# Kernel optimization log

Hardware: AMD Instinct MI355X
Metric: run time of the kernel (lower is better)

## Reference

```python
import jax, jax.numpy as jnp
import numpy as np

B, C, H, W = 8, 256, 128, 128
K = 3  # conv kernel size, padding=1 -> SAME


def conv3x3(x, w, b):
    # x: [B,C,H,W], w: [O,I,K,K], b: [O]
    y = jax.lax.conv_general_dilated(
        x, w, window_strides=(1, 1), padding='SAME',
        dimension_numbers=('NCHW', 'OIHW', 'NCHW'))
    return y + b[None, :, None, None]


def setup_inputs() -> dict:
    key = jax.random.key(0)
    ks = jax.random.split(key, 7)
    fan_in = C * K * K
    s = 1.0 / np.sqrt(fan_in)
    x = jax.random.normal(ks[0], (B, C, H, W), dtype=jnp.float32)
    Wq = jax.random.uniform(ks[1], (C, C, K, K), jnp.float32, -s, s)
    bq = jax.random.uniform(ks[2], (C,), jnp.float32, -s, s)
    Wk = jax.random.uniform(ks[3], (C, C, K, K), jnp.float32, -s, s)
    bk = jax.random.uniform(ks[4], (C,), jnp.float32, -s, s)
    Wv = jax.random.uniform(ks[5], (C, C, K, K), jnp.float32, -s, s)
    bv = jax.random.uniform(ks[6], (C,), jnp.float32, -s, s)
    return {'x': x, 'Wq': Wq, 'bq': bq, 'Wk': Wk, 'bk': bk, 'Wv': Wv, 'bv': bv}


def reference(x, Wq, bq, Wk, bk, Wv, bv):
    b_, c_, h_, w_ = x.shape
    residual = x
    q = jax.nn.relu(conv3x3(x, Wq, bq))  # [B,C,H,W]
    k = jax.nn.relu(conv3x3(x, Wk, bk))  # [B,C,H,W]
    v = conv3x3(x, Wv, bv)               # [B,C,H,W]
    # per-(batch,channel) spatial matmul: [H,W] @ [H,W] -> [H,W] (requires H==W)
    attn = jnp.einsum('bcij,bcjk->bcik', q, k)
    # softmax over the flattened H*W positions jointly per (b,c)
    attn = jax.nn.softmax(attn.reshape(b_, c_, h_ * w_), axis=-1).reshape(b_, c_, h_, w_)
    y = jnp.einsum('bcij,bcjk->bcik', attn, v)
    return y + residual
```

## Files before the change

### kernel.cpp

```cpp
#include <hip/hip_runtime.h>

#define BB 8
#define CC 256
#define HH 128
#define WW 128
#define HW (HH*WW)

typedef float f32x4 __attribute__((ext_vector_type(4)));
typedef float f32x16 __attribute__((ext_vector_type(16)));
typedef short s16x8 __attribute__((ext_vector_type(8)));

__device__ inline unsigned short f2bf(float f) {
  union { float f; unsigned int u; } un;
  un.f = f;
  unsigned int u = un.u;
  return (unsigned short)((u + 0x7fffu + ((u >> 16) & 1u)) >> 16);
}

__device__ __forceinline__ void gload_lds16(const void* g, void* l) {
  __builtin_amdgcn_global_load_lds(
      (const __attribute__((address_space(1))) unsigned int*)g,
      (__attribute__((address_space(3))) unsigned int*)l, 16, 0, 0);
}

__global__ __launch_bounds__(256) void k_prepass(const float* __restrict__ x,
                                                 unsigned short* __restrict__ xbf) {
  __shared__ float tile[64][68];
  int bh = blockIdx.x;
  int b = bh >> 7, h = bh & 127;
  int w0 = blockIdx.y * 64;
  int c0 = blockIdx.z * 64;
  int t = threadIdx.x;
  {
    int c = t >> 2, wq = (t & 3) << 4;
    const float4* src = reinterpret_cast<const float4*>(
        x + (((size_t)(b * CC + c0 + c) * HH + h) * WW + w0 + wq));
    float4 v0 = src[0], v1 = src[1], v2 = src[2], v3 = src[3];
    *reinterpret_cast<float4*>(&tile[c][wq + 0])  = v0;
    *reinterpret_cast<float4*>(&tile[c][wq + 4])  = v1;
    *reinterpret_cast<float4*>(&tile[c][wq + 8])  = v2;
    *reinterpret_cast<float4*>(&tile[c][wq + 12]) = v3;
  }
  __syncthreads();
  {
    int w = t >> 2, cg = (t & 3) << 4;
    unsigned short tmp[16];
#pragma unroll
    for (int i = 0; i < 16; ++i) tmp[i] = f2bf(tile[cg + i][w]);
    unsigned short* dst = xbf + ((size_t)(b * HH + h) * WW + w0 + w) * CC + c0 + cg;
    *reinterpret_cast<int4*>(dst)     = *reinterpret_cast<int4*>(tmp);
    *reinterpret_cast<int4*>(dst + 8) = *reinterpret_cast<int4*>(tmp + 8);
  }
}

__global__ __launch_bounds__(256) void k_repack(const float* __restrict__ Wq,
                                                const float* __restrict__ Wk,
                                                const float* __restrict__ Wv,
                                                unsigned short* __restrict__ Wp,
                                                unsigned short* __restrict__ zp) {
  if (blockIdx.x == 0 && threadIdx.x < 64) {
    int4 z = {0, 0, 0, 0};
    reinterpret_cast<int4*>(zp)[threadIdx.x] = z;
  }
  int idx = blockIdx.x * 256 + threadIdx.x;
  if (idx >= 8 * 9 * 768 * 32) return;
  int ci = idx & 31;
  int tmp = idx >> 5;
  int focs = tmp % 768;
  int tmp2 = tmp / 768;
  int tap = tmp2 % 9;
  int chunk = tmp2 / 9;
  int cv = focs >> 8, oc = focs & 255;
  int cin = chunk * 32 + ci;
  const float* Wsrc = (cv == 0) ? Wq : ((cv == 1) ? Wk : Wv);
  Wp[idx] = f2bf(Wsrc[(size_t)(oc * 256 + cin) * 9 + tap]);
}

__global__ __launch_bounds__(256, 2) void k_conv(const unsigned short* __restrict__ xbf,
                                                 const unsigned short* __restrict__ Wp,
                                                 const unsigned short* __restrict__ zp,
                                                 const float* __restrict__ bq,
                                                 const float* __restrict__ bk,
                                                 const float* __restrict__ bv,
                                                 unsigned short* __restrict__ qkv) {
  __shared__ unsigned short xs[2][4][132][32];
  __shared__ float bias_s[128];
  int bid = blockIdx.x;
  int v_ = (bid & 7) * 384 + (bid >> 3);
  int mtile = v_ % 6;
  int bhp = v_ / 6;
  int b = bhp >> 6;
  int h0 = (bhp & 63) * 2;
  int t = threadIdx.x;
  int lane = t & 63, wave = t >> 6;
  int wm = wave >> 1, wq = wave & 1;
  int l31 = lane & 31, lg1 = lane >> 5;

  if (t < 128) {
    int focs = mtile * 128 + t;
    int cv = focs >> 8, oc = focs & 255;
    const float* bp = (cv == 0) ? bq : ((cv == 1) ? bk : bv);
    bias_s[t] = bp[oc];
  }
  {
    int cell = t >> 4;
    int bf_ = cell >> 3, r_ = (cell >> 1) & 3;
    int wc_ = (cell & 1) ? 129 : 0;
    *reinterpret_cast<int*>(reinterpret_cast<char*>(&xs[bf_][r_][wc_][0]) + (t & 15) * 4) = 0;
  }

  int l2 = lane >> 2, l4 = lane & 3;
  int osw = l4 ^ (((l2 + 1) >> 1) & 3);
  int hin = h0 + wave - 1;
  bool inb = ((unsigned)hin < 128u);
  const unsigned short* srow =
      xbf + ((size_t)(b * HH + (inb ? hin : 0)) * WW + l2) * CC + osw * 8;
  const unsigned short* zsrc = zp + lane * 8;

  const size_t CH_STRIDE = (size_t)9 * 768 * 32;
  const unsigned short* apbase = Wp + (size_t)(mtile * 128 + wm * 64 + l31) * 32 + lg1 * 8;

  f32x16 acc[2][2][2] = {};
  s16x8 Afb[2][3][2];

  {
    char* d0 = reinterpret_cast<char*>(&xs[0][wave][1][0]);
    if (inb) {
#pragma unroll
      for (int j = 0; j < 8; ++j) gload_lds16(srow + j * (16 * CC), d0 + j * 1024);
    } else {
#pragma unroll
      for (int j = 0; j < 8; ++j) gload_lds16(zsrc, d0 + j * 1024);
    }
  }
#pragma unroll
  for (int rr = 0; rr < 3; ++rr)
#pragma unroll
  for (int mt = 0; mt < 2; ++mt)
    Afb[0][rr][mt] = *reinterpret_cast<const s16x8*>(apbase + (rr * 3) * (768 * 32) + mt * 1024);
  __syncthreads();

  for (int chunk = 0; chunk < 8; ++chunk) {
    const int buf = chunk & 1;
    const unsigned short* ap_cur = apbase + chunk * CH_STRIDE;
    const unsigned short* ap_nxt = (chunk < 7) ? ap_cur + CH_STRIDE : ap_cur;
    const char* xsb = reinterpret_cast<const char*>(&xs[buf][0][0][0]);
    char* dstg = reinterpret_cast<char*>(&xs[buf ^ 1][wave][1][0]);
    const unsigned short* sstg = srow + (chunk + 1) * 32;

#pragma unroll
    for (int p = 0; p < 6; ++p) {
      const int ss = p >> 1, kk = p & 1;
      s16x8 Bf[4][2];
#pragma unroll
      for (int rin = 0; rin < 4; ++rin)
#pragma unroll
      for (int nt = 0; nt < 2; ++nt) {
        int wc = wq * 64 + nt * 32 + l31 + ss;
        int pslot = (kk * 2 + lg1) ^ ((wc >> 1) & 3);
        Bf[rin][nt] = *reinterpret_cast<const s16x8*>(
            xsb + rin * (132 * 64) + wc * 64 + pslot * 16);
      }
      {
        const int pn = (p + 1) % 6, ssn = pn >> 1, kkn = pn & 1;
        const unsigned short* apn = (p == 5) ? ap_nxt : ap_cur;
#pragma unroll
        for (int rr = 0; rr < 3; ++rr)
#pragma unroll
        for (int mt = 0; mt < 2; ++mt)
          Afb[(p + 1) & 1][rr][mt] = *reinterpret_cast<const s16x8*>(
              apn + (rr * 3 + ssn) * (768 * 32) + mt * 1024 + kkn * 16);
      }
      __builtin_amdgcn_sched_barrier(0);
      if (p < 4 && chunk < 7) {
        if (inb) {
          gload_lds16(sstg + (2 * p) * (16 * CC), dstg + (2 * p) * 1024);
          gload_lds16(sstg + (2 * p + 1) * (16 * CC), dstg + (2 * p + 1) * 1024);
        } else {
          gload_lds16(zsrc, dstg + (2 * p) * 1024);
          gload_lds16(zsrc, dstg + (2 * p + 1) * 1024);
        }
      }
      __builtin_amdgcn_sched_barrier(0);
      __builtin_amdgcn_s_setprio(1);
#pragma unroll
      for (int rr = 0; rr < 3; ++rr)
#pragma unroll
      for (int row = 0; row < 2; ++row)
#pragma unroll
      for (int mt = 0; mt < 2; ++mt)
#pragma unroll
      for (int nt = 0; nt < 2; ++nt)
        acc[mt][row][nt] = __builtin_amdgcn_mfma_f32_32x32x16_bf16(
            Afb[p & 1][rr][mt], Bf[row + rr][nt], acc[mt][row][nt], 0, 0, 0);
      __builtin_amdgcn_s_setprio(0);
      __builtin_amdgcn_sched_barrier(0);
    }
    if (chunk < 7) {
      asm volatile("s_waitcnt vmcnt(12)" ::: "memory");
      __builtin_amdgcn_s_barrier();
      asm volatile("" ::: "memory");
      __builtin_amdgcn_sched_barrier(0);
    }
  }

#pragma unroll
  for (int mt = 0; mt < 2; ++mt) {
#pragma unroll
    for (int row = 0; row < 2; ++row) {
#pragma unroll
      for (int nt = 0; nt < 2; ++nt) {
        int wcol = wq * 64 + nt * 32 + l31;
        int h = h0 + row;
#pragma unroll
        for (int reg = 0; reg < 16; ++reg) {
          int rloc = (reg & 3) + 8 * (reg >> 2) + 4 * lg1;
          int floc = wm * 64 + mt * 32 + rloc;
          float vv = acc[mt][row][nt][reg] + bias_s[floc];
          int focs = mtile * 128 + floc;
          if (focs < 512) vv = fmaxf(vv, 0.0f);
          int cv = focs >> 8, oc = focs & 255;
          qkv[(size_t)(cv * 2048 + b * 256 + oc) * HW + h * WW + wcol] = f2bf(vv);
        }
      }
    }
  }
}

#define PADA 136
__global__ __launch_bounds__(256) void k_attn(const unsigned short* __restrict__ qkv,
                                              const float* __restrict__ x,
                                              float* __restrict__ out) {
  __shared__ unsigned short al[128][PADA];
  __shared__ unsigned short kt[128][PADA];
  __shared__ unsigned short vt[128][PADA];
  __shared__ float red[8];
  int bc = blockIdx.x;
  const unsigned short* qp = qkv + (size_t)bc * HW;
  const unsigned short* kp = qkv + (size_t)(2048 + bc) * HW;
  const unsigned short* vp = qkv + (size_t)(4096 + bc) * HW;
  int t = threadIdx.x;
  for (int g = t; g < HW; g += 256) {
    int row = g >> 7, col = g & 127;
    kt[col][row] = kp[g];
    vt[col][row] = vp[g];
  }
  __syncthreads();
  int lane = t & 63, wave = t >> 6;
  int wm = wave >> 1, wn = wave & 1;
  int l15 = lane & 15, lg = lane >> 4;
  f32x4 acc[4][4] = {};
#pragma unroll
  for (int kk = 0; kk < 4; ++kk) {
    s16x8 af[4], bfr[4];
#pragma unroll
    for (int m = 0; m < 4; ++m)
      af[m] = *reinterpret_cast<const s16x8*>(qp + (size_t)(wm * 64 + m * 16 + l15) * WW + kk * 32 + lg * 8);
#pragma unroll
    for (int n = 0; n < 4; ++n)
      bfr[n] = *reinterpret_cast<const s16x8*>(&kt[wn * 64 + n * 16 + l15][kk * 32 + lg * 8]);
#pragma unroll
    for (int m = 0; m < 4; ++m)
#pragma unroll
      for (int n = 0; n < 4; ++n)
        acc[m][n] = __builtin_amdgcn_mfma_f32_16x16x32_bf16(af[m], bfr[n], acc[m][n], 0, 0, 0);
  }
  float lm = -3.0e38f;
#pragma unroll
  for (int m = 0; m < 4; ++m)
#pragma unroll
    for (int n = 0; n < 4; ++n)
#pragma unroll
      for (int rg = 0; rg < 4; ++rg)
        lm = fmaxf(lm, acc[m][n][rg]);
  for (int off = 32; off > 0; off >>= 1) lm = fmaxf(lm, __shfl_xor(lm, off));
  if (lane == 0) red[wave] = lm;
  __syncthreads();
  float M = fmaxf(fmaxf(red[0], red[1]), fmaxf(red[2], red[3]));
  float ls = 0.0f;
#pragma unroll
  for (int m = 0; m < 4; ++m)
#pragma unroll
    for (int n = 0; n < 4; ++n)
#pragma unroll
      for (int rg = 0; rg < 4; ++rg)
        ls += __expf(acc[m][n][rg] - M);
  for (int off = 32; off > 0; off >>= 1) ls += __shfl_xor(ls, off);
  if (lane == 0) red[4 + wave] = ls;
  __syncthreads();
  float inv = 1.0f / (red[4] + red[5] + red[6] + red[7]);
#pragma unroll
  for (int m = 0; m < 4; ++m) {
#pragma unroll
    for (int n = 0; n < 4; ++n) {
      int col = wn * 64 + n * 16 + l15;
#pragma unroll
      for (int rg = 0; rg < 4; ++rg) {
        int row = wm * 64 + m * 16 + lg * 4 + rg;
        al[row][col] = f2bf(__expf(acc[m][n][rg] - M) * inv);
      }
    }
  }
  __syncthreads();
  f32x4 o_[4][4] = {};
#pragma unroll
  for (int kk = 0; kk < 4; ++kk) {
    s16x8 af[4], bfr[4];
#pragma unroll
    for (int m = 0; m < 4; ++m)
      af[m] = *reinterpret_cast<const s16x8*>(&al[wm * 64 + m * 16 + l15][kk * 32 + lg * 8]);
#pragma unroll
    for (int n = 0; n < 4; ++n)
      bfr[n] = *reinterpret_cast<const s16x8*>(&vt[wn * 64 + n * 16 + l15][kk * 32 + lg * 8]);
#pragma unroll
    for (int m = 0; m < 4; ++m)
#pragma unroll
      for (int n = 0; n < 4; ++n)
        o_[m][n] = __builtin_amdgcn_mfma_f32_16x16x32_bf16(af[m], bfr[n], o_[m][n], 0, 0, 0);
  }
  const float* xp = x + (size_t)bc * HW;
  float* op = out + (size_t)bc * HW;
#pragma unroll
  for (int m = 0; m < 4; ++m) {
#pragma unroll
    for (int n = 0; n < 4; ++n) {
      int col = wn * 64 + n * 16 + l15;
#pragma unroll
      for (int rg = 0; rg < 4; ++rg) {
        int row = wm * 64 + m * 16 + lg * 4 + rg;
        op[row * WW + col] = o_[m][n][rg] + xp[row * WW + col];
      }
    }
  }
}

extern "C" void kernel_launch(void* const* d_in, const int* in_sizes, int n_in,
                              void* d_out, int out_size, void* d_ws, size_t ws_size,
                              hipStream_t stream) {
  const float* x  = (const float*)d_in[0];
  const float* Wq = (const float*)d_in[1];
  const float* bq = (const float*)d_in[2];
  const float* Wk = (const float*)d_in[3];
  const float* bk = (const float*)d_in[4];
  const float* Wv = (const float*)d_in[5];
  const float* bv = (const float*)d_in[6];
  float* out = (float*)d_out;

  unsigned short* xbf = (unsigned short*)d_ws;
  unsigned short* qkv = xbf + (size_t)33554432;
  unsigned short* Wp  = qkv + (size_t)3 * 33554432;
  unsigned short* zp  = Wp + (size_t)(8 * 9 * 768 * 32);

  dim3 g0(1024, 2, 4);
  k_prepass<<<g0, 256, 0, stream>>>(x, xbf);
  k_repack<<<6912, 256, 0, stream>>>(Wq, Wk, Wv, Wp, zp);
  k_conv<<<3072, 256, 0, stream>>>(xbf, Wp, zp, bq, bk, bv, qkv);
  k_attn<<<2048, 256, 0, stream>>>(qkv, x, out);
}
```

Before: 606.1 us.

## Reassign conv waves to 32-filter by full-width tiles with pipelined B-fragment loads

Changes the conv kernel's wave decomposition from a 2x2 grid (64 filters x 64 columns per wave) to 4 waves each owning 32 filters across all 128 columns. Each wave now loads fewer weight fragments and reads more LDS activation fragments, which are software-pipelined one column tile ahead and interleaved with the MFMAs. This aims to cut global weight-load traffic and register pressure and to overlap LDS reads with compute. In exchange LDS read volume per wave rises, and the wait count before each barrier is adjusted.

```diff
diff --git a/kernel.cpp b/kernel.cpp
--- a/kernel.cpp
+++ b/kernel.cpp
@@ -93,7 +93,7 @@
   int h0 = (bhp & 63) * 2;
   int t = threadIdx.x;
   int lane = t & 63, wave = t >> 6;
-  int wm = wave >> 1, wq = wave & 1;
+  int fq = wave;
   int l31 = lane & 31, lg1 = lane >> 5;
 
   if (t < 128) {
@@ -118,110 +118,109 @@
   const unsigned short* zsrc = zp + lane * 8;
 
   const size_t CH_STRIDE = (size_t)9 * 768 * 32;
-  const unsigned short* apbase = Wp + (size_t)(mtile * 128 + wm * 64 + l31) * 32 + lg1 * 8;
-
-  f32x16 acc[2][2][2] = {};
-  s16x8 Afb[2][3][2];
-
-  {
-    char* d0 = reinterpret_cast<char*>(&xs[0][wave][1][0]);
+  const unsigned short* apbase = Wp + (size_t)(mtile * 128 + fq * 32 + l31) * 32 + lg1 * 8;
+
+  auto STAGE = [&](int bufn, int c) {
+    char* d0 = reinterpret_cast<char*>(&xs[bufn][wave][1][0]);
     if (inb) {
-#pragma unroll
-      for (int j = 0; j < 8; ++j) gload_lds16(srow + j * (16 * CC), d0 + j * 1024);
+      const unsigned short* s0 = srow + c * 32;
+#pragma unroll
+      for (int j = 0; j < 8; ++j) gload_lds16(s0 + j * (16 * CC), d0 + j * 1024);
     } else {
 #pragma unroll
       for (int j = 0; j < 8; ++j) gload_lds16(zsrc, d0 + j * 1024);
     }
-  }
-#pragma unroll
-  for (int rr = 0; rr < 3; ++rr)
-#pragma unroll
-  for (int mt = 0; mt < 2; ++mt)
-    Afb[0][rr][mt] = *reinterpret_cast<const s16x8*>(apbase + (rr * 3) * (768 * 32) + mt * 1024);
-  __syncthreads();
+  };
+  auto ALOAD = [&](s16x8 (&Af)[3], const unsigned short* ap, int un) {
+    const int ss = un >> 1, kk = un & 1;
+#pragma unroll
+    for (int rr = 0; rr < 3; ++rr)
+      Af[rr] = *reinterpret_cast<const s16x8*>(ap + (rr * 3 + ss) * (768 * 32) + kk * 16);
+  };
+  auto BREAD = [&](s16x8 (&Bf)[4], const char* xsb, int un, int nt) {
+    const int ss = un >> 1, kk = un & 1;
+    const int col = nt * 32 + l31 + ss;
+    const int pslot = (kk * 2 + lg1) ^ ((col >> 1) & 3);
+#pragma unroll
+    for (int rin = 0; rin < 4; ++rin)
+      Bf[rin] = *reinterpret_cast<const s16x8*>(
+          xsb + rin * (132 * 64) + col * 64 + pslot * 16);
+  };
+
+  f32x16 acc[2][4] = {};
+  s16x8 Afb[2][3];
+  s16x8 Bfb[2][4];
+
+  STAGE(0, 0);
+  ALOAD(Afb[0], apbase, 0);
+  asm volatile("s_waitcnt vmcnt(3)" ::: "memory");
+  __builtin_amdgcn_s_barrier();
+  BREAD(Bfb[0], reinterpret_cast<const char*>(&xs[0][0][0][0]), 0, 0);
 
   for (int chunk = 0; chunk < 8; ++chunk) {
     const int buf = chunk & 1;
     const unsigned short* ap_cur = apbase + chunk * CH_STRIDE;
-    const unsigned short* ap_nxt = (chunk < 7) ? ap_cur + CH_STRIDE : ap_cur;
     const char* xsb = reinterpret_cast<const char*>(&xs[buf][0][0][0]);
-    char* dstg = reinterpret_cast<char*>(&xs[buf ^ 1][wave][1][0]);
-    const unsigned short* sstg = srow + (chunk + 1) * 32;
-
-#pragma unroll
-    for (int p = 0; p < 6; ++p) {
-      const int ss = p >> 1, kk = p & 1;
-      s16x8 Bf[4][2];
-#pragma unroll
-      for (int rin = 0; rin < 4; ++rin)
-#pragma unroll
-      for (int nt = 0; nt < 2; ++nt) {
-        int wc = wq * 64 + nt * 32 + l31 + ss;
-        int pslot = (kk * 2 + lg1) ^ ((wc >> 1) & 3);
-        Bf[rin][nt] = *reinterpret_cast<const s16x8*>(
-            xsb + rin * (132 * 64) + wc * 64 + pslot * 16);
+
+#pragma unroll
+    for (int u = 0; u < 6; ++u) {
+#pragma unroll
+      for (int nt = 0; nt < 4; ++nt) {
+        if (nt < 3) {
+          BREAD(Bfb[(nt + 1) & 1], xsb, u, nt + 1);
+        } else if (u < 5) {
+          BREAD(Bfb[0], xsb, u + 1, 0);
+        }
+        if (nt == 0) {
+          if (u < 5) ALOAD(Afb[(u + 1) & 1], ap_cur, u + 1);
+          else if (chunk < 7) ALOAD(Afb[0], ap_cur + CH_STRIDE, 0);
+          if (u < 4 && chunk < 7) {
+            char* dstg = reinterpret_cast<char*>(&xs[buf ^ 1][wave][1][0]);
+            if (inb) {
+              const unsigned short* s0 = srow + (chunk + 1) * 32;
+              gload_lds16(s0 + (2 * u) * (16 * CC), dstg + (2 * u) * 1024);
+              gload_lds16(s0 + (2 * u + 1) * (16 * CC), dstg + (2 * u + 1) * 1024);
+            } else {
+              gload_lds16(zsrc, dstg + (2 * u) * 1024);
+              gload_lds16(zsrc, dstg + (2 * u + 1) * 1024);
+            }
+          }
+        }
+        __builtin_amdgcn_sched_barrier(0);
+        __builtin_amdgcn_s_setprio(1);
+#pragma unroll
+        for (int rr = 0; rr < 3; ++rr)
+#pragma unroll
+          for (int row = 0; row < 2; ++row)
+            acc[row][nt] = __builtin_amdgcn_mfma_f32_32x32x16_bf16(
+                Afb[u & 1][rr], Bfb[nt & 1][row + rr], acc[row][nt], 0, 0, 0);
+        __builtin_amdgcn_s_setprio(0);
+        __builtin_amdgcn_sched_barrier(0);
       }
-      {
-        const int pn = (p + 1) % 6, ssn = pn >> 1, kkn = pn & 1;
-        const unsigned short* apn = (p == 5) ? ap_nxt : ap_cur;
-#pragma unroll
-        for (int rr = 0; rr < 3; ++rr)
-#pragma unroll
-        for (int mt = 0; mt < 2; ++mt)
-          Afb[(p + 1) & 1][rr][mt] = *reinterpret_cast<const s16x8*>(
-              apn + (rr * 3 + ssn) * (768 * 32) + mt * 1024 + kkn * 16);
-      }
-      __builtin_amdgcn_sched_barrier(0);
-      if (p < 4 && chunk < 7) {
-        if (inb) {
-          gload_lds16(sstg + (2 * p) * (16 * CC), dstg + (2 * p) * 1024);
-          gload_lds16(sstg + (2 * p + 1) * (16 * CC), dstg + (2 * p + 1) * 1024);
-        } else {
-          gload_lds16(zsrc, dstg + (2 * p) * 1024);
-          gload_lds16(zsrc, dstg + (2 * p + 1) * 1024);
-        }
-      }
-      __builtin_amdgcn_sched_barrier(0);
-      __builtin_amdgcn_s_setprio(1);
-#pragma unroll
-      for (int rr = 0; rr < 3; ++rr)
-#pragma unroll
-      for (int row = 0; row < 2; ++row)
-#pragma unroll
-      for (int mt = 0; mt < 2; ++mt)
-#pragma unroll
-      for (int nt = 0; nt < 2; ++nt)
-        acc[mt][row][nt] = __builtin_amdgcn_mfma_f32_32x32x16_bf16(
-            Afb[p & 1][rr][mt], Bf[row + rr][nt], acc[mt][row][nt], 0, 0, 0);
-      __builtin_amdgcn_s_setprio(0);
-      __builtin_amdgcn_sched_barrier(0);
     }
     if (chunk < 7) {
-      asm volatile("s_waitcnt vmcnt(12)" ::: "memory");
+      asm volatile("s_waitcnt vmcnt(6)" ::: "memory");
       __builtin_amdgcn_s_barrier();
       asm volatile("" ::: "memory");
-      __builtin_amdgcn_sched_barrier(0);
-    }
-  }
-
-#pragma unroll
-  for (int mt = 0; mt < 2; ++mt) {
-#pragma unroll
-    for (int row = 0; row < 2; ++row) {
-#pragma unroll
-      for (int nt = 0; nt < 2; ++nt) {
-        int wcol = wq * 64 + nt * 32 + l31;
-        int h = h0 + row;
-#pragma unroll
-        for (int reg = 0; reg < 16; ++reg) {
-          int rloc = (reg & 3) + 8 * (reg >> 2) + 4 * lg1;
-          int floc = wm * 64 + mt * 32 + rloc;
-          float vv = acc[mt][row][nt][reg] + bias_s[floc];
-          int focs = mtile * 128 + floc;
-          if (focs < 512) vv = fmaxf(vv, 0.0f);
-          int cv = focs >> 8, oc = focs & 255;
-          qkv[(size_t)(cv * 2048 + b * 256 + oc) * HW + h * WW + wcol] = f2bf(vv);
-        }
+      BREAD(Bfb[0], reinterpret_cast<const char*>(&xs[buf ^ 1][0][0][0]), 0, 0);
+    }
+  }
+
+#pragma unroll
+  for (int row = 0; row < 2; ++row) {
+#pragma unroll
+    for (int nt = 0; nt < 4; ++nt) {
+      int wcol = nt * 32 + l31;
+      int h = h0 + row;
+#pragma unroll
+      for (int reg = 0; reg < 16; ++reg) {
+        int rloc = (reg & 3) + 8 * (reg >> 2) + 4 * lg1;
+        int floc = fq * 32 + rloc;
+        float vv = acc[row][nt][reg] + bias_s[floc];
+        int focs = mtile * 128 + floc;
+        if (focs < 512) vv = fmaxf(vv, 0.0f);
+        int cv = focs >> 8, oc = focs & 255;
+        qkv[(size_t)(cv * 2048 + b * 256 + oc) * HW + h * WW + wcol] = f2bf(vv);
       }
     }
   }
```

Result: faster. 557.9 us (-8.0%).
